# Optimization experiments

Hardware: AMD Instinct MI355X
Metric: run time of the kernel (lower is better)

Reference implementation:

```python
import jax, jax.numpy as jnp
import numpy as np

LENGTH, D, CHI, CLASSES = 784, 2, 128, 10
BATCH = 1024


def setup_inputs() -> dict:
    key = jax.random.key(0)
    k1, k2, k3 = jax.random.split(key, 3)
    # feature-mapped samples (batch, d, length), values in [0,1] like cossin map
    x = jax.random.uniform(k1, (BATCH, D, LENGTH), dtype=jnp.float32)
    # per-site residual weights; small init so the residual recurrence stays stable
    W = jax.random.normal(k2, (LENGTH, D, CHI, CHI), dtype=jnp.float32) * (0.01 / np.sqrt(CHI))
    # classifier matrix applied to the final hidden vector
    V = jax.random.normal(k3, (CHI, CLASSES), dtype=jnp.float32) / np.sqrt(CHI)
    return {"x": x, "W": W, "V": V}


def reference(x, W, V):
    # x: (B, d, L), W: (L, d, chi, chi), V: (chi, classes)
    B = x.shape[0]
    chi = W.shape[2]
    h0 = jnp.ones((B, chi), dtype=x.dtype)  # initial hidden bond vector

    xs = jnp.moveaxis(x, 2, 0)  # (L, B, d) so scan iterates over sites

    def site_step(h, inputs):
        xn, Wn = inputs  # xn: (B, d), Wn: (d, chi, chi)
        # residual MPS update: h <- h + sum_{s,a} x[n,s] W_n[s,a,b] h[a]
        h = h + jnp.einsum('ns,sab,na->nb', xn, Wn, h)
        return h, None

    h, _ = jax.lax.scan(site_step, h0, (xs, W))
    logits = h @ V  # (B, classes)
    return logits
```

## Files before the change

kernel.cpp:

```cpp
#include <hip/hip_runtime.h>

#define LL 784
#define CHI 128
#define CLS 10
#define BC 16
#define NBLK 64

typedef __attribute__((ext_vector_type(8))) short short8;
typedef __attribute__((ext_vector_type(4))) float floatx4;

__device__ inline unsigned int f2bf(float v) {
    unsigned int u = __float_as_uint(v);
    u += 0x7fffu + ((u >> 16) & 1u);
    return u >> 16;
}

__device__ inline void lds_barrier() {
    asm volatile("s_waitcnt lgkmcnt(0)\n\ts_barrier" ::: "memory");
}

__device__ inline unsigned int cvt_pk_bf16(float lo, float hi) {
    unsigned int r;
    asm("v_cvt_pk_bf16_f32 %0, %1, %2" : "=v"(r) : "v"(lo), "v"(hi));
    return r;
}

template <int OFF>
__device__ inline short8 gload(const char* p) {
    short8 r;
    asm volatile("global_load_dwordx4 %0, %1, off offset:%2"
                 : "=v"(r) : "v"(p), "i"(OFF));
    return r;
}

__device__ inline floatx4 gloadf4(const float* p) {
    floatx4 r;
    asm volatile("global_load_dwordx4 %0, %1, off"
                 : "=v"(r) : "v"(p));
    return r;
}

__device__ inline void vm_wait24() {
    asm volatile("s_waitcnt vmcnt(24)" ::: "memory");
    __builtin_amdgcn_sched_barrier(0);
}
__device__ inline void vm_wait16() {
    asm volatile("s_waitcnt vmcnt(16)" ::: "memory");
    __builtin_amdgcn_sched_barrier(0);
}
__device__ inline void vm_wait8() {
    asm volatile("s_waitcnt vmcnt(8)" ::: "memory");
    __builtin_amdgcn_sched_barrier(0);
}
__device__ inline void vm_wait0() {
    asm volatile("s_waitcnt vmcnt(0)" ::: "memory");
    __builtin_amdgcn_sched_barrier(0);
}

__global__ __launch_bounds__(256) void prep_kernel(const float* __restrict__ W,
                                                   uint4* __restrict__ ws4) {
    __shared__ float tile[32 * 132];
    const int b = blockIdx.x;
    const int n = b >> 3, s = (b >> 2) & 1, kt = b & 3;
    const float* Wp = W + ((size_t)(n * 2 + s) * CHI + kt * 32) * CHI;
    const int t = threadIdx.x;
    #pragma unroll
    for (int k = 0; k < 4; k++) {
        int v = t + k * 256;
        int a = v >> 5, c4 = v & 31;
        float4 val = *(const float4*)(Wp + a * CHI + c4 * 4);
        *(float4*)&tile[a * 132 + c4 * 4] = val;
    }
    __syncthreads();
    const int l = t & 63, f0 = t >> 6;
    const int m_ = l & 15, q_ = l >> 4;
    #pragma unroll
    for (int ff = 0; ff < 2; ff++) {
        int nt = f0 + ff * 4;
        const float* tp = &tile[(q_ * 8) * 132 + nt * 16 + m_];
        uint4 pk;
        pk.x = f2bf(tp[0 * 132]) | (f2bf(tp[1 * 132]) << 16);
        pk.y = f2bf(tp[2 * 132]) | (f2bf(tp[3 * 132]) << 16);
        pk.z = f2bf(tp[4 * 132]) | (f2bf(tp[5 * 132]) << 16);
        pk.w = f2bf(tp[6 * 132]) | (f2bf(tp[7 * 132]) << 16);
        ws4[(size_t)(((n * 8 + nt) * 2 + s) * 4 + kt) * 64 + l] = pk;
    }
}

__global__ __launch_bounds__(512) void mps_kernel(const float* __restrict__ x,
                                                  const unsigned short* __restrict__ ws,
                                                  const float* __restrict__ V,
                                                  float* __restrict__ out) {
    __shared__ short8 bfbuf[2][4][64];
    __shared__ float hfin[BC * 136];

    const int t = threadIdx.x;
    const int w = t >> 6, l = t & 63;
    const int m = l & 15, q = l >> 4;
    const int rb = blockIdx.x * BC;

    for (int i = t; i < 1024; i += 512)
        ((unsigned int*)&bfbuf[0][0][0])[i] = 0x3F803F80u;

    const float* xp0 = x + (size_t)(rb + m) * (2 * LL);
    const float* xp1 = xp0 + LL;
    floatx4 xA0, xA1, xA2, xA3, xB0, xB1, xB2, xB3;
    xA0 = gloadf4(xp0 + 0);  xA1 = gloadf4(xp0 + 4);
    xA2 = gloadf4(xp1 + 0);  xA3 = gloadf4(xp1 + 4);

    const char* wsb = (const char*)ws + (size_t)w * 8192 + (size_t)l * 16;

    short8 bWA[8], bWB[8], bWC[8], bWD[8];
#define LOAD_BATCH(BUF, PTR) do {                                   \
    const char* p_ = (PTR);                                         \
    BUF[0] = gload<0>(p_);           BUF[1] = gload<1024>(p_);      \
    BUF[2] = gload<2048>(p_);        BUF[3] = gload<3072>(p_);      \
    BUF[4] = gload<0>(p_ + 4096);    BUF[5] = gload<1024>(p_ + 4096); \
    BUF[6] = gload<2048>(p_ + 4096); BUF[7] = gload<3072>(p_ + 4096); \
} while (0)

    LOAD_BATCH(bWA, wsb);
    LOAD_BATCH(bWB, wsb + 1 * 65536);
    LOAD_BATCH(bWC, wsb + 2 * 65536);
    LOAD_BATCH(bWD, wsb + 3 * 65536);

    floatx4 hacc = (floatx4){1.f, 1.f, 1.f, 1.f};

    unsigned int* const bfw = (unsigned int*)&bfbuf[0][0][0];
    const int wr_dw = (w >> 1) * 256 + (m + 16 * ((w & 1) * 2 + (q >> 1))) * 4 + (q & 1) * 2;

    __syncthreads();

#define SITE_BODY(NN, PAR, WBUF, X0, X1, PF, WAIT) do {                             \
    lds_barrier();                                                                  \
    short8 bf0 = bfbuf[PAR][0][l];                                                  \
    short8 bf1 = bfbuf[PAR][1][l];                                                  \
    short8 bf2 = bfbuf[PAR][2][l];                                                  \
    short8 bf3 = bfbuf[PAR][3][l];                                                  \
    WAIT();                                                                         \
    floatx4 z = (floatx4){0.f, 0.f, 0.f, 0.f};                                      \
    floatx4 p0 = __builtin_amdgcn_mfma_f32_16x16x32_bf16(WBUF[0], bf0, z, 0, 0, 0); \
    floatx4 p1 = __builtin_amdgcn_mfma_f32_16x16x32_bf16(WBUF[2], bf2, z, 0, 0, 0); \
    floatx4 q0 = __builtin_amdgcn_mfma_f32_16x16x32_bf16(WBUF[4], bf0, z, 0, 0, 0); \
    floatx4 q1 = __builtin_amdgcn_mfma_f32_16x16x32_bf16(WBUF[6], bf2, z, 0, 0, 0); \
    p0 = __builtin_amdgcn_mfma_f32_16x16x32_bf16(WBUF[1], bf1, p0, 0, 0, 0);        \
    p1 = __builtin_amdgcn_mfma_f32_16x16x32_bf16(WBUF[3], bf3, p1, 0, 0, 0);        \
    q0 = __builtin_amdgcn_mfma_f32_16x16x32_bf16(WBUF[5], bf1, q0, 0, 0, 0);        \
    q1 = __builtin_amdgcn_mfma_f32_16x16x32_bf16(WBUF[7], bf3, q1, 0, 0, 0);        \
    if (PF) LOAD_BATCH(WBUF, wsb + (size_t)((NN) + 4) * 65536);                     \
    _Pragma("unroll")                                                               \
    for (int i = 0; i < 4; i++)                                                     \
        hacc[i] += (X0) * (p0[i] + p1[i]) + (X1) * (q0[i] + q1[i]);                 \
    uint2 pk;                                                                       \
    pk.x = cvt_pk_bf16(hacc[0], hacc[1]);                                           \
    pk.y = cvt_pk_bf16(hacc[2], hacc[3]);                                           \
    *(uint2*)&bfw[((PAR) ^ 1) * 1024 + wr_dw] = pk;                                 \
} while (0)

    for (int nb = 0; nb < LL - 16; nb += 16) {
        xB0 = gloadf4(xp0 + nb + 8);
        xB1 = gloadf4(xp0 + nb + 12);
        xB2 = gloadf4(xp1 + nb + 8);
        xB3 = gloadf4(xp1 + nb + 12);
        SITE_BODY(nb + 0,  0, bWA, xA0[0], xA2[0], 1, vm_wait24);
        SITE_BODY(nb + 1,  1, bWB, xA0[1], xA2[1], 1, vm_wait24);
        SITE_BODY(nb + 2,  0, bWC, xA0[2], xA2[2], 1, vm_wait24);
        SITE_BODY(nb + 3,  1, bWD, xA0[3], xA2[3], 1, vm_wait24);
        SITE_BODY(nb + 4,  0, bWA, xA1[0], xA3[0], 1, vm_wait24);
        SITE_BODY(nb + 5,  1, bWB, xA1[1], xA3[1], 1, vm_wait24);
        SITE_BODY(nb + 6,  0, bWC, xA1[2], xA3[2], 1, vm_wait24);
        SITE_BODY(nb + 7,  1, bWD, xA1[3], xA3[3], 1, vm_wait24);
        xA0 = gloadf4(xp0 + nb + 16);
        xA1 = gloadf4(xp0 + nb + 20);
        xA2 = gloadf4(xp1 + nb + 16);
        xA3 = gloadf4(xp1 + nb + 20);
        SITE_BODY(nb + 8,  0, bWA, xB0[0], xB2[0], 1, vm_wait24);
        SITE_BODY(nb + 9,  1, bWB, xB0[1], xB2[1], 1, vm_wait24);
        SITE_BODY(nb + 10, 0, bWC, xB0[2], xB2[2], 1, vm_wait24);
        SITE_BODY(nb + 11, 1, bWD, xB0[3], xB2[3], 1, vm_wait24);
        SITE_BODY(nb + 12, 0, bWA, xB1[0], xB3[0], 1, vm_wait24);
        SITE_BODY(nb + 13, 1, bWB, xB1[1], xB3[1], 1, vm_wait24);
        SITE_BODY(nb + 14, 0, bWC, xB1[2], xB3[2], 1, vm_wait24);
        SITE_BODY(nb + 15, 1, bWD, xB1[3], xB3[3], 1, vm_wait24);
    }

    xB0 = gloadf4(xp0 + 768 + 8);
    xB1 = gloadf4(xp0 + 768 + 12);
    xB2 = gloadf4(xp1 + 768 + 8);
    xB3 = gloadf4(xp1 + 768 + 12);
    SITE_BODY(768, 0, bWA, xA0[0], xA2[0], 1, vm_wait24);
    SITE_BODY(769, 1, bWB, xA0[1], xA2[1], 1, vm_wait24);
    SITE_BODY(770, 0, bWC, xA0[2], xA2[2], 1, vm_wait24);
    SITE_BODY(771, 1, bWD, xA0[3], xA2[3], 1, vm_wait24);
    SITE_BODY(772, 0, bWA, xA1[0], xA3[0], 1, vm_wait24);
    SITE_BODY(773, 1, bWB, xA1[1], xA3[1], 1, vm_wait24);
    SITE_BODY(774, 0, bWC, xA1[2], xA3[2], 1, vm_wait24);
    SITE_BODY(775, 1, bWD, xA1[3], xA3[3], 1, vm_wait24);
    SITE_BODY(776, 0, bWA, xB0[0], xB2[0], 1, vm_wait24);
    SITE_BODY(777, 1, bWB, xB0[1], xB2[1], 1, vm_wait24);
    SITE_BODY(778, 0, bWC, xB0[2], xB2[2], 1, vm_wait24);
    SITE_BODY(779, 1, bWD, xB0[3], xB2[3], 1, vm_wait24);
    SITE_BODY(780, 0, bWA, xB1[0], xB3[0], 0, vm_wait24);
    SITE_BODY(781, 1, bWB, xB1[1], xB3[1], 0, vm_wait16);
    SITE_BODY(782, 0, bWC, xB1[2], xB3[2], 0, vm_wait8);
    SITE_BODY(783, 1, bWD, xB1[3], xB3[3], 0, vm_wait0);
#undef SITE_BODY
#undef LOAD_BATCH

    *(floatx4*)&hfin[m * 136 + w * 16 + q * 4] = hacc;
    __syncthreads();

    if (t < BC * CLS) {
        int r = t / CLS, cls = t % CLS;
        float sum = 0.f;
        for (int a = 0; a < CHI; a++) sum += hfin[r * 136 + a] * V[a * CLS + cls];
        out[(size_t)(rb + r) * CLS + cls] = sum;
    }
}

extern "C" void kernel_launch(void* const* d_in, const int* in_sizes, int n_in,
                              void* d_out, int out_size, void* d_ws, size_t ws_size,
                              hipStream_t stream) {
    const float* x = (const float*)d_in[0];
    const float* W = (const float*)d_in[1];
    const float* V = (const float*)d_in[2];
    float* out = (float*)d_out;

    prep_kernel<<<LL * 8, 256, 0, stream>>>(W, (uint4*)d_ws);
    mps_kernel<<<NBLK, 512, 0, stream>>>(x, (const unsigned short*)d_ws, V, out);
}
```

Measured before the change: 682.5 us.

## Process 32 batch rows per block, sharing each site's weight loads across two tiles

Each block now handles two 16-row batch tiles, so every weight fragment loaded from global memory feeds twice as many MFMAs. The grid halves from 64 to 32 blocks. The weight prefetch depth drops from four sites to two, which frees registers for the second accumulator and x buffers. The trade-off is that only half as many CUs are busy, each with longer per-site compute, and the shallower prefetch leaves less time to hide weight-load latency on the serial recurrence.

Result: slower. 843.7 us (+23.6%).

```diff
diff --git a/kernel.cpp b/kernel.cpp
--- a/kernel.cpp
+++ b/kernel.cpp
@@ -3,8 +3,8 @@
 #define LL 784
 #define CHI 128
 #define CLS 10
-#define BC 16
-#define NBLK 64
+#define BC 32
+#define NBLK 32
 
 typedef __attribute__((ext_vector_type(8))) short short8;
 typedef __attribute__((ext_vector_type(4))) float floatx4;
@@ -40,14 +40,6 @@
     return r;
 }
 
-__device__ inline void vm_wait24() {
-    asm volatile("s_waitcnt vmcnt(24)" ::: "memory");
-    __builtin_amdgcn_sched_barrier(0);
-}
-__device__ inline void vm_wait16() {
-    asm volatile("s_waitcnt vmcnt(16)" ::: "memory");
-    __builtin_amdgcn_sched_barrier(0);
-}
 __device__ inline void vm_wait8() {
     asm volatile("s_waitcnt vmcnt(8)" ::: "memory");
     __builtin_amdgcn_sched_barrier(0);
@@ -91,7 +83,7 @@
                                                   const unsigned short* __restrict__ ws,
                                                   const float* __restrict__ V,
                                                   float* __restrict__ out) {
-    __shared__ short8 bfbuf[2][4][64];
+    __shared__ short8 bfbuf[2][4][2][64];
     __shared__ float hfin[BC * 136];
 
     const int t = threadIdx.x;
@@ -99,18 +91,23 @@
     const int m = l & 15, q = l >> 4;
     const int rb = blockIdx.x * BC;
 
-    for (int i = t; i < 1024; i += 512)
-        ((unsigned int*)&bfbuf[0][0][0])[i] = 0x3F803F80u;
+    for (int i = t; i < 2048; i += 512)
+        ((unsigned int*)&bfbuf[0][0][0][0])[i] = 0x3F803F80u;
 
     const float* xp0 = x + (size_t)(rb + m) * (2 * LL);
     const float* xp1 = xp0 + LL;
+    const float* xp2 = x + (size_t)(rb + 16 + m) * (2 * LL);
+    const float* xp3 = xp2 + LL;
     floatx4 xA0, xA1, xA2, xA3, xB0, xB1, xB2, xB3;
+    floatx4 xC0, xC1, xC2, xC3, xD0, xD1, xD2, xD3;
     xA0 = gloadf4(xp0 + 0);  xA1 = gloadf4(xp0 + 4);
     xA2 = gloadf4(xp1 + 0);  xA3 = gloadf4(xp1 + 4);
+    xC0 = gloadf4(xp2 + 0);  xC1 = gloadf4(xp2 + 4);
+    xC2 = gloadf4(xp3 + 0);  xC3 = gloadf4(xp3 + 4);
 
     const char* wsb = (const char*)ws + (size_t)w * 8192 + (size_t)l * 16;
 
-    short8 bWA[8], bWB[8], bWC[8], bWD[8];
+    short8 bWA[8], bWB[8];
 #define LOAD_BATCH(BUF, PTR) do {                                   \
     const char* p_ = (PTR);                                         \
     BUF[0] = gload<0>(p_);           BUF[1] = gload<1024>(p_);      \
@@ -120,41 +117,58 @@
 } while (0)
 
     LOAD_BATCH(bWA, wsb);
-    LOAD_BATCH(bWB, wsb + 1 * 65536);
-    LOAD_BATCH(bWC, wsb + 2 * 65536);
-    LOAD_BATCH(bWD, wsb + 3 * 65536);
-
-    floatx4 hacc = (floatx4){1.f, 1.f, 1.f, 1.f};
-
-    unsigned int* const bfw = (unsigned int*)&bfbuf[0][0][0];
-    const int wr_dw = (w >> 1) * 256 + (m + 16 * ((w & 1) * 2 + (q >> 1))) * 4 + (q & 1) * 2;
+    LOAD_BATCH(bWB, wsb + 65536);
+
+    floatx4 hacc0 = (floatx4){1.f, 1.f, 1.f, 1.f};
+    floatx4 hacc1 = (floatx4){1.f, 1.f, 1.f, 1.f};
+
+    unsigned int* const bfw = (unsigned int*)&bfbuf[0][0][0][0];
+    const int l2 = m + 16 * ((w & 1) * 2 + (q >> 1));
+    const int wr_dw = ((w >> 1) * 2) * 256 + l2 * 4 + (q & 1) * 2;
 
     __syncthreads();
 
-#define SITE_BODY(NN, PAR, WBUF, X0, X1, PF, WAIT) do {                             \
-    lds_barrier();                                                                  \
-    short8 bf0 = bfbuf[PAR][0][l];                                                  \
-    short8 bf1 = bfbuf[PAR][1][l];                                                  \
-    short8 bf2 = bfbuf[PAR][2][l];                                                  \
-    short8 bf3 = bfbuf[PAR][3][l];                                                  \
-    WAIT();                                                                         \
-    floatx4 z = (floatx4){0.f, 0.f, 0.f, 0.f};                                      \
-    floatx4 p0 = __builtin_amdgcn_mfma_f32_16x16x32_bf16(WBUF[0], bf0, z, 0, 0, 0); \
-    floatx4 p1 = __builtin_amdgcn_mfma_f32_16x16x32_bf16(WBUF[2], bf2, z, 0, 0, 0); \
-    floatx4 q0 = __builtin_amdgcn_mfma_f32_16x16x32_bf16(WBUF[4], bf0, z, 0, 0, 0); \
-    floatx4 q1 = __builtin_amdgcn_mfma_f32_16x16x32_bf16(WBUF[6], bf2, z, 0, 0, 0); \
-    p0 = __builtin_amdgcn_mfma_f32_16x16x32_bf16(WBUF[1], bf1, p0, 0, 0, 0);        \
-    p1 = __builtin_amdgcn_mfma_f32_16x16x32_bf16(WBUF[3], bf3, p1, 0, 0, 0);        \
-    q0 = __builtin_amdgcn_mfma_f32_16x16x32_bf16(WBUF[5], bf1, q0, 0, 0, 0);        \
-    q1 = __builtin_amdgcn_mfma_f32_16x16x32_bf16(WBUF[7], bf3, q1, 0, 0, 0);        \
-    if (PF) LOAD_BATCH(WBUF, wsb + (size_t)((NN) + 4) * 65536);                     \
-    _Pragma("unroll")                                                               \
-    for (int i = 0; i < 4; i++)                                                     \
-        hacc[i] += (X0) * (p0[i] + p1[i]) + (X1) * (q0[i] + q1[i]);                 \
-    uint2 pk;                                                                       \
-    pk.x = cvt_pk_bf16(hacc[0], hacc[1]);                                           \
-    pk.y = cvt_pk_bf16(hacc[2], hacc[3]);                                           \
-    *(uint2*)&bfw[((PAR) ^ 1) * 1024 + wr_dw] = pk;                                 \
+#define SITE_BODY(NN, PAR, WBUF, X0, X1, X2, X3, PF, WAIT) do {                       \
+    lds_barrier();                                                                    \
+    short8 bf00 = bfbuf[PAR][0][0][l];                                                \
+    short8 bf10 = bfbuf[PAR][1][0][l];                                                \
+    short8 bf20 = bfbuf[PAR][2][0][l];                                                \
+    short8 bf30 = bfbuf[PAR][3][0][l];                                                \
+    short8 bf01 = bfbuf[PAR][0][1][l];                                                \
+    short8 bf11 = bfbuf[PAR][1][1][l];                                                \
+    short8 bf21 = bfbuf[PAR][2][1][l];                                                \
+    short8 bf31 = bfbuf[PAR][3][1][l];                                                \
+    WAIT();                                                                           \
+    floatx4 z = (floatx4){0.f, 0.f, 0.f, 0.f};                                        \
+    floatx4 pA0 = __builtin_amdgcn_mfma_f32_16x16x32_bf16(WBUF[0], bf00, z, 0, 0, 0); \
+    floatx4 pA1 = __builtin_amdgcn_mfma_f32_16x16x32_bf16(WBUF[2], bf20, z, 0, 0, 0); \
+    floatx4 qA0 = __builtin_amdgcn_mfma_f32_16x16x32_bf16(WBUF[4], bf00, z, 0, 0, 0); \
+    floatx4 qA1 = __builtin_amdgcn_mfma_f32_16x16x32_bf16(WBUF[6], bf20, z, 0, 0, 0); \
+    floatx4 pB0 = __builtin_amdgcn_mfma_f32_16x16x32_bf16(WBUF[0], bf01, z, 0, 0, 0); \
+    floatx4 pB1 = __builtin_amdgcn_mfma_f32_16x16x32_bf16(WBUF[2], bf21, z, 0, 0, 0); \
+    floatx4 qB0 = __builtin_amdgcn_mfma_f32_16x16x32_bf16(WBUF[4], bf01, z, 0, 0, 0); \
+    floatx4 qB1 = __builtin_amdgcn_mfma_f32_16x16x32_bf16(WBUF[6], bf21, z, 0, 0, 0); \
+    pA0 = __builtin_amdgcn_mfma_f32_16x16x32_bf16(WBUF[1], bf10, pA0, 0, 0, 0);       \
+    pA1 = __builtin_amdgcn_mfma_f32_16x16x32_bf16(WBUF[3], bf30, pA1, 0, 0, 0);       \
+    qA0 = __builtin_amdgcn_mfma_f32_16x16x32_bf16(WBUF[5], bf10, qA0, 0, 0, 0);       \
+    qA1 = __builtin_amdgcn_mfma_f32_16x16x32_bf16(WBUF[7], bf30, qA1, 0, 0, 0);       \
+    pB0 = __builtin_amdgcn_mfma_f32_16x16x32_bf16(WBUF[1], bf11, pB0, 0, 0, 0);       \
+    pB1 = __builtin_amdgcn_mfma_f32_16x16x32_bf16(WBUF[3], bf31, pB1, 0, 0, 0);       \
+    qB0 = __builtin_amdgcn_mfma_f32_16x16x32_bf16(WBUF[5], bf11, qB0, 0, 0, 0);       \
+    qB1 = __builtin_amdgcn_mfma_f32_16x16x32_bf16(WBUF[7], bf31, qB1, 0, 0, 0);       \
+    if (PF) LOAD_BATCH(WBUF, wsb + (size_t)((NN) + 2) * 65536);                       \
+    _Pragma("unroll")                                                                 \
+    for (int i = 0; i < 4; i++) {                                                     \
+        hacc0[i] += (X0) * (pA0[i] + pA1[i]) + (X1) * (qA0[i] + qA1[i]);              \
+        hacc1[i] += (X2) * (pB0[i] + pB1[i]) + (X3) * (qB0[i] + qB1[i]);              \
+    }                                                                                 \
+    uint2 pk0, pk1;                                                                   \
+    pk0.x = cvt_pk_bf16(hacc0[0], hacc0[1]);                                          \
+    pk0.y = cvt_pk_bf16(hacc0[2], hacc0[3]);                                          \
+    pk1.x = cvt_pk_bf16(hacc1[0], hacc1[1]);                                          \
+    pk1.y = cvt_pk_bf16(hacc1[2], hacc1[3]);                                          \
+    *(uint2*)&bfw[((PAR) ^ 1) * 2048 + wr_dw]       = pk0;                            \
+    *(uint2*)&bfw[((PAR) ^ 1) * 2048 + 256 + wr_dw] = pk1;                            \
 } while (0)
 
     for (int nb = 0; nb < LL - 16; nb += 16) {
@@ -162,52 +176,65 @@
         xB1 = gloadf4(xp0 + nb + 12);
         xB2 = gloadf4(xp1 + nb + 8);
         xB3 = gloadf4(xp1 + nb + 12);
-        SITE_BODY(nb + 0,  0, bWA, xA0[0], xA2[0], 1, vm_wait24);
-        SITE_BODY(nb + 1,  1, bWB, xA0[1], xA2[1], 1, vm_wait24);
-        SITE_BODY(nb + 2,  0, bWC, xA0[2], xA2[2], 1, vm_wait24);
-        SITE_BODY(nb + 3,  1, bWD, xA0[3], xA2[3], 1, vm_wait24);
-        SITE_BODY(nb + 4,  0, bWA, xA1[0], xA3[0], 1, vm_wait24);
-        SITE_BODY(nb + 5,  1, bWB, xA1[1], xA3[1], 1, vm_wait24);
-        SITE_BODY(nb + 6,  0, bWC, xA1[2], xA3[2], 1, vm_wait24);
-        SITE_BODY(nb + 7,  1, bWD, xA1[3], xA3[3], 1, vm_wait24);
+        xD0 = gloadf4(xp2 + nb + 8);
+        xD1 = gloadf4(xp2 + nb + 12);
+        xD2 = gloadf4(xp3 + nb + 8);
+        xD3 = gloadf4(xp3 + nb + 12);
+        SITE_BODY(nb + 0,  0, bWA, xA0[0], xA2[0], xC0[0], xC2[0], 1, vm_wait8);
+        SITE_BODY(nb + 1,  1, bWB, xA0[1], xA2[1], xC0[1], xC2[1], 1, vm_wait8);
+        SITE_BODY(nb + 2,  0, bWA, xA0[2], xA2[2], xC0[2], xC2[2], 1, vm_wait8);
+        SITE_BODY(nb + 3,  1, bWB, xA0[3], xA2[3], xC0[3], xC2[3], 1, vm_wait8);
+        SITE_BODY(nb + 4,  0, bWA, xA1[0], xA3[0], xC1[0], xC3[0], 1, vm_wait8);
+        SITE_BODY(nb + 5,  1, bWB, xA1[1], xA3[1], xC1[1], xC3[1], 1, vm_wait8);
+        SITE_BODY(nb + 6,  0, bWA, xA1[2], xA3[2], xC1[2], xC3[2], 1, vm_wait8);
+        SITE_BODY(nb + 7,  1, bWB, xA1[3], xA3[3], xC1[3], xC3[3], 1, vm_wait8);
         xA0 = gloadf4(xp0 + nb + 16);
         xA1 = gloadf4(xp0 + nb + 20);
         xA2 = gloadf4(xp1 + nb + 16);
         xA3 = gloadf4(xp1 + nb + 20);
-        SITE_BODY(nb + 8,  0, bWA, xB0[0], xB2[0], 1, vm_wait24);
-        SITE_BODY(nb + 9,  1, bWB, xB0[1], xB2[1], 1, vm_wait24);
-        SITE_BODY(nb + 10, 0, bWC, xB0[2], xB2[2], 1, vm_wait24);
-        SITE_BODY(nb + 11, 1, bWD, xB0[3], xB2[3], 1, vm_wait24);
-        SITE_BODY(nb + 12, 0, bWA, xB1[0], xB3[0], 1, vm_wait24);
-        SITE_BODY(nb + 13, 1, bWB, xB1[1], xB3[1], 1, vm_wait24);
-        SITE_BODY(nb + 14, 0, bWC, xB1[2], xB3[2], 1, vm_wait24);
-        SITE_BODY(nb + 15, 1, bWD, xB1[3], xB3[3], 1, vm_wait24);
+        xC0 = gloadf4(xp2 + nb + 16);
+        xC1 = gloadf4(xp2 + nb + 20);
+        xC2 = gloadf4(xp3 + nb + 16);
+        xC3 = gloadf4(xp3 + nb + 20);
+        SITE_BODY(nb + 8,  0, bWA, xB0[0], xB2[0], xD0[0], xD2[0], 1, vm_wait8);
+        SITE_BODY(nb + 9,  1, bWB, xB0[1], xB2[1], xD0[1], xD2[1], 1, vm_wait8);
+        SITE_BODY(nb + 10, 0, bWA, xB0[2], xB2[2], xD0[2], xD2[2], 1, vm_wait8);
+        SITE_BODY(nb + 11, 1, bWB, xB0[3], xB2[3], xD0[3], xD2[3], 1, vm_wait8);
+        SITE_BODY(nb + 12, 0, bWA, xB1[0], xB3[0], xD1[0], xD3[0], 1, vm_wait8);
+        SITE_BODY(nb + 13, 1, bWB, xB1[1], xB3[1], xD1[1], xD3[1], 1, vm_wait8);
+        SITE_BODY(nb + 14, 0, bWA, xB1[2], xB3[2], xD1[2], xD3[2], 1, vm_wait8);
+        SITE_BODY(nb + 15, 1, bWB, xB1[3], xB3[3], xD1[3], xD3[3], 1, vm_wait8);
     }
 
     xB0 = gloadf4(xp0 + 768 + 8);
     xB1 = gloadf4(xp0 + 768 + 12);
     xB2 = gloadf4(xp1 + 768 + 8);
     xB3 = gloadf4(xp1 + 768 + 12);
-    SITE_BODY(768, 0, bWA, xA0[0], xA2[0], 1, vm_wait24);
-    SITE_BODY(769, 1, bWB, xA0[1], xA2[1], 1, vm_wait24);
-    SITE_BODY(770, 0, bWC, xA0[2], xA2[2], 1, vm_wait24);
-    SITE_BODY(771, 1, bWD, xA0[3], xA2[3], 1, vm_wait24);
-    SITE_BODY(772, 0, bWA, xA1[0], xA3[0], 1, vm_wait24);
-    SITE_BODY(773, 1, bWB, xA1[1], xA3[1], 1, vm_wait24);
-    SITE_BODY(774, 0, bWC, xA1[2], xA3[2], 1, vm_wait24);
-    SITE_BODY(775, 1, bWD, xA1[3], xA3[3], 1, vm_wait24);
-    SITE_BODY(776, 0, bWA, xB0[0], xB2[0], 1, vm_wait24);
-    SITE_BODY(777, 1, bWB, xB0[1], xB2[1], 1, vm_wait24);
-    SITE_BODY(778, 0, bWC, xB0[2], xB2[2], 1, vm_wait24);
-    SITE_BODY(779, 1, bWD, xB0[3], xB2[3], 1, vm_wait24);
-    SITE_BODY(780, 0, bWA, xB1[0], xB3[0], 0, vm_wait24);
-    SITE_BODY(781, 1, bWB, xB1[1], xB3[1], 0, vm_wait16);
-    SITE_BODY(782, 0, bWC, xB1[2], xB3[2], 0, vm_wait8);
-    SITE_BODY(783, 1, bWD, xB1[3], xB3[3], 0, vm_wait0);
+    xD0 = gloadf4(xp2 + 768 + 8);
+    xD1 = gloadf4(xp2 + 768 + 12);
+    xD2 = gloadf4(xp3 + 768 + 8);
+    xD3 = gloadf4(xp3 + 768 + 12);
+    SITE_BODY(768, 0, bWA, xA0[0], xA2[0], xC0[0], xC2[0], 1, vm_wait8);
+    SITE_BODY(769, 1, bWB, xA0[1], xA2[1], xC0[1], xC2[1], 1, vm_wait8);
+    SITE_BODY(770, 0, bWA, xA0[2], xA2[2], xC0[2], xC2[2], 1, vm_wait8);
+    SITE_BODY(771, 1, bWB, xA0[3], xA2[3], xC0[3], xC2[3], 1, vm_wait8);
+    SITE_BODY(772, 0, bWA, xA1[0], xA3[0], xC1[0], xC3[0], 1, vm_wait8);
+    SITE_BODY(773, 1, bWB, xA1[1], xA3[1], xC1[1], xC3[1], 1, vm_wait8);
+    SITE_BODY(774, 0, bWA, xA1[2], xA3[2], xC1[2], xC3[2], 1, vm_wait8);
+    SITE_BODY(775, 1, bWB, xA1[3], xA3[3], xC1[3], xC3[3], 1, vm_wait8);
+    SITE_BODY(776, 0, bWA, xB0[0], xB2[0], xD0[0], xD2[0], 1, vm_wait8);
+    SITE_BODY(777, 1, bWB, xB0[1], xB2[1], xD0[1], xD2[1], 1, vm_wait8);
+    SITE_BODY(778, 0, bWA, xB0[2], xB2[2], xD0[2], xD2[2], 1, vm_wait8);
+    SITE_BODY(779, 1, bWB, xB0[3], xB2[3], xD0[3], xD2[3], 1, vm_wait8);
+    SITE_BODY(780, 0, bWA, xB1[0], xB3[0], xD1[0], xD3[0], 1, vm_wait8);
+    SITE_BODY(781, 1, bWB, xB1[1], xB3[1], xD1[1], xD3[1], 1, vm_wait8);
+    SITE_BODY(782, 0, bWA, xB1[2], xB3[2], xD1[2], xD3[2], 0, vm_wait8);
+    SITE_BODY(783, 1, bWB, xB1[3], xB3[3], xD1[3], xD3[3], 0, vm_wait0);
 #undef SITE_BODY
 #undef LOAD_BATCH
 
-    *(floatx4*)&hfin[m * 136 + w * 16 + q * 4] = hacc;
+    *(floatx4*)&hfin[m * 136 + w * 16 + q * 4]        = hacc0;
+    *(floatx4*)&hfin[(m + 16) * 136 + w * 16 + q * 4] = hacc1;
     __syncthreads();
 
     if (t < BC * CLS) {
```

## Switch recurrence matmuls to FP8 MFMA with residual decomposition around ones

Applied to the files above, without the earlier changes.

Quantizes W (scaled by 256) to FP8 E4M3 and stores h as FP8 offsets from the all-ones start vector (scaled by 16). The ones contribution is handled exactly through precomputed column sums R produced by a new prep kernel. Each site now uses eight FP8 MFMAs with half-size weight loads and a two-deep prefetch instead of four. This halves weight bandwidth and register footprint. In exchange it adds software FP8 conversion on the critical path, one more kernel, and more quantization error.

Result: slower. 774.9 us (+13.5%).

```diff
diff --git a/kernel.cpp b/kernel.cpp
--- a/kernel.cpp
+++ b/kernel.cpp
@@ -6,33 +6,43 @@
 #define BC 16
 #define NBLK 64
 
-typedef __attribute__((ext_vector_type(8))) short short8;
 typedef __attribute__((ext_vector_type(4))) float floatx4;
-
-__device__ inline unsigned int f2bf(float v) {
+typedef __attribute__((ext_vector_type(2))) long lng2;
+
+__device__ inline unsigned int f2fp8(float v) {
     unsigned int u = __float_as_uint(v);
-    u += 0x7fffu + ((u >> 16) & 1u);
-    return u >> 16;
+    unsigned int s = (u >> 24) & 0x80u;
+    unsigned int a = u & 0x7fffffffu;
+    if (a >= 0x43e00000u) return s | 0x7Eu;
+    if (a <  0x3c800000u) return s;
+    unsigned int r = a + 0x0007ffffu + ((a >> 20) & 1u);
+    if (r >= 0x43e00000u) return s | 0x7Eu;
+    unsigned int E = (r >> 23) - 120u;
+    return s | (E << 3) | ((r >> 20) & 7u);
+}
+
+__device__ inline unsigned int pk4_fp8(float v0, float v1, float v2, float v3) {
+    return f2fp8(v0) | (f2fp8(v1) << 8) | (f2fp8(v2) << 16) | (f2fp8(v3) << 24);
 }
 
 __device__ inline void lds_barrier() {
     asm volatile("s_waitcnt lgkmcnt(0)\n\ts_barrier" ::: "memory");
 }
 
-__device__ inline unsigned int cvt_pk_bf16(float lo, float hi) {
-    unsigned int r;
-    asm("v_cvt_pk_bf16_f32 %0, %1, %2" : "=v"(r) : "v"(lo), "v"(hi));
-    return r;
-}
-
 template <int OFF>
-__device__ inline short8 gload(const char* p) {
-    short8 r;
+__device__ inline lng2 gload16(const char* p) {
+    lng2 r;
     asm volatile("global_load_dwordx4 %0, %1, off offset:%2"
                  : "=v"(r) : "v"(p), "i"(OFF));
     return r;
 }
-
+template <int OFF>
+__device__ inline floatx4 gloadf4o(const float* p) {
+    floatx4 r;
+    asm volatile("global_load_dwordx4 %0, %1, off offset:%2"
+                 : "=v"(r) : "v"(p), "i"(OFF));
+    return r;
+}
 __device__ inline floatx4 gloadf4(const float* p) {
     floatx4 r;
     asm volatile("global_load_dwordx4 %0, %1, off"
@@ -40,16 +50,12 @@
     return r;
 }
 
-__device__ inline void vm_wait24() {
-    asm volatile("s_waitcnt vmcnt(24)" ::: "memory");
+__device__ inline void vm_wait10() {
+    asm volatile("s_waitcnt vmcnt(10)" ::: "memory");
     __builtin_amdgcn_sched_barrier(0);
 }
-__device__ inline void vm_wait16() {
-    asm volatile("s_waitcnt vmcnt(16)" ::: "memory");
-    __builtin_amdgcn_sched_barrier(0);
-}
-__device__ inline void vm_wait8() {
-    asm volatile("s_waitcnt vmcnt(8)" ::: "memory");
+__device__ inline void vm_wait6() {
+    asm volatile("s_waitcnt vmcnt(6)" ::: "memory");
     __builtin_amdgcn_sched_barrier(0);
 }
 __device__ inline void vm_wait0() {
@@ -58,7 +64,7 @@
 }
 
 __global__ __launch_bounds__(256) void prep_kernel(const float* __restrict__ W,
-                                                   uint4* __restrict__ ws4) {
+                                                   unsigned char* __restrict__ ws8) {
     __shared__ float tile[32 * 132];
     const int b = blockIdx.x;
     const int n = b >> 3, s = (b >> 2) & 1, kt = b & 3;
@@ -74,24 +80,39 @@
     __syncthreads();
     const int l = t & 63, f0 = t >> 6;
     const int m_ = l & 15, q_ = l >> 4;
+    const int f = s * 4 + kt;
     #pragma unroll
     for (int ff = 0; ff < 2; ff++) {
         int nt = f0 + ff * 4;
         const float* tp = &tile[(q_ * 8) * 132 + nt * 16 + m_];
-        uint4 pk;
-        pk.x = f2bf(tp[0 * 132]) | (f2bf(tp[1 * 132]) << 16);
-        pk.y = f2bf(tp[2 * 132]) | (f2bf(tp[3 * 132]) << 16);
-        pk.z = f2bf(tp[4 * 132]) | (f2bf(tp[5 * 132]) << 16);
-        pk.w = f2bf(tp[6 * 132]) | (f2bf(tp[7 * 132]) << 16);
-        ws4[(size_t)(((n * 8 + nt) * 2 + s) * 4 + kt) * 64 + l] = pk;
-    }
+        unsigned int dw0 = pk4_fp8(tp[0 * 132] * 256.f, tp[1 * 132] * 256.f,
+                                   tp[2 * 132] * 256.f, tp[3 * 132] * 256.f);
+        unsigned int dw1 = pk4_fp8(tp[4 * 132] * 256.f, tp[5 * 132] * 256.f,
+                                   tp[6 * 132] * 256.f, tp[7 * 132] * 256.f);
+        size_t addr = (size_t)n * 32768 + (size_t)nt * 4096 + (f >> 1) * 1024
+                    + l * 16 + (f & 1) * 8;
+        uint2 pk; pk.x = dw0; pk.y = dw1;
+        *(uint2*)(ws8 + addr) = pk;
+    }
+}
+
+__global__ __launch_bounds__(256) void prepR_kernel(const float* __restrict__ W,
+                                                    float* __restrict__ R) {
+    const int n = blockIdx.x, t = threadIdx.x;
+    const int s = t >> 7, c = t & 127;
+    const float* Wp = W + ((size_t)(n * 2 + s) * CHI) * CHI + c;
+    float sum = 0.f;
+    #pragma unroll 8
+    for (int a = 0; a < CHI; a++) sum += Wp[(size_t)a * CHI];
+    R[(n * 2 + s) * CHI + c] = sum;
 }
 
 __global__ __launch_bounds__(512) void mps_kernel(const float* __restrict__ x,
-                                                  const unsigned short* __restrict__ ws,
+                                                  const unsigned char* __restrict__ ws8,
+                                                  const float* __restrict__ R,
                                                   const float* __restrict__ V,
                                                   float* __restrict__ out) {
-    __shared__ short8 bfbuf[2][4][64];
+    __shared__ long bfb[2][4][64];
     __shared__ float hfin[BC * 136];
 
     const int t = threadIdx.x;
@@ -99,8 +120,7 @@
     const int m = l & 15, q = l >> 4;
     const int rb = blockIdx.x * BC;
 
-    for (int i = t; i < 1024; i += 512)
-        ((unsigned int*)&bfbuf[0][0][0])[i] = 0x3F803F80u;
+    for (int i = t; i < 256; i += 512) ((long*)bfb)[i] = 0L;
 
     const float* xp0 = x + (size_t)(rb + m) * (2 * LL);
     const float* xp1 = xp0 + LL;
@@ -108,53 +128,56 @@
     xA0 = gloadf4(xp0 + 0);  xA1 = gloadf4(xp0 + 4);
     xA2 = gloadf4(xp1 + 0);  xA3 = gloadf4(xp1 + 4);
 
-    const char* wsb = (const char*)ws + (size_t)w * 8192 + (size_t)l * 16;
-
-    short8 bWA[8], bWB[8], bWC[8], bWD[8];
-#define LOAD_BATCH(BUF, PTR) do {                                   \
-    const char* p_ = (PTR);                                         \
-    BUF[0] = gload<0>(p_);           BUF[1] = gload<1024>(p_);      \
-    BUF[2] = gload<2048>(p_);        BUF[3] = gload<3072>(p_);      \
-    BUF[4] = gload<0>(p_ + 4096);    BUF[5] = gload<1024>(p_ + 4096); \
-    BUF[6] = gload<2048>(p_ + 4096); BUF[7] = gload<3072>(p_ + 4096); \
+    const char* wsb = (const char*)ws8 + (size_t)w * 4096 + (size_t)l * 16;
+    const float* rbase = R + w * 16 + q * 4;
+
+    lng2 bWA[4], bWB[4];
+    floatx4 rA0, rA1, rB0, rB1;
+#define LOAD_BATCH(WB_, R0_, R1_, NT_) do {                         \
+    const char* p_ = wsb + (size_t)(NT_) * 32768;                   \
+    WB_[0] = gload16<0>(p_);     WB_[1] = gload16<1024>(p_);        \
+    WB_[2] = gload16<2048>(p_);  WB_[3] = gload16<3072>(p_);        \
+    const float* rp_ = rbase + (NT_) * 256;                         \
+    R0_ = gloadf4o<0>(rp_);  R1_ = gloadf4o<512>(rp_);              \
 } while (0)
 
-    LOAD_BATCH(bWA, wsb);
-    LOAD_BATCH(bWB, wsb + 1 * 65536);
-    LOAD_BATCH(bWC, wsb + 2 * 65536);
-    LOAD_BATCH(bWD, wsb + 3 * 65536);
+    LOAD_BATCH(bWA, rA0, rA1, 0);
+    LOAD_BATCH(bWB, rB0, rB1, 1);
 
     floatx4 hacc = (floatx4){1.f, 1.f, 1.f, 1.f};
 
-    unsigned int* const bfw = (unsigned int*)&bfbuf[0][0][0];
-    const int wr_dw = (w >> 1) * 256 + (m + 16 * ((w & 1) * 2 + (q >> 1))) * 4 + (q & 1) * 2;
+    unsigned int* const bfw = (unsigned int*)&bfb[0][0][0];
+    const int wr_dw = (w >> 1) * 128 + (m + 16 * ((w & 1) * 2 + (q >> 1))) * 2 + (q & 1);
 
     __syncthreads();
 
-#define SITE_BODY(NN, PAR, WBUF, X0, X1, PF, WAIT) do {                             \
+#define MFMA8(A, B, C) __builtin_amdgcn_mfma_f32_16x16x32_fp8_fp8((A), (B), (C), 0, 0, 0)
+
+#define SITE_BODY(NN, PAR, WBUF, RB0_, RB1_, X0, X1, PF, WAIT) do {                 \
     lds_barrier();                                                                  \
-    short8 bf0 = bfbuf[PAR][0][l];                                                  \
-    short8 bf1 = bfbuf[PAR][1][l];                                                  \
-    short8 bf2 = bfbuf[PAR][2][l];                                                  \
-    short8 bf3 = bfbuf[PAR][3][l];                                                  \
+    long d0 = bfb[PAR][0][l];                                                       \
+    long d1 = bfb[PAR][1][l];                                                       \
+    long d2 = bfb[PAR][2][l];                                                       \
+    long d3 = bfb[PAR][3][l];                                                       \
     WAIT();                                                                         \
+    floatx4 r0 = RB0_, r1 = RB1_;                \
     floatx4 z = (floatx4){0.f, 0.f, 0.f, 0.f};                                      \
-    floatx4 p0 = __builtin_amdgcn_mfma_f32_16x16x32_bf16(WBUF[0], bf0, z, 0, 0, 0); \
-    floatx4 p1 = __builtin_amdgcn_mfma_f32_16x16x32_bf16(WBUF[2], bf2, z, 0, 0, 0); \
-    floatx4 q0 = __builtin_amdgcn_mfma_f32_16x16x32_bf16(WBUF[4], bf0, z, 0, 0, 0); \
-    floatx4 q1 = __builtin_amdgcn_mfma_f32_16x16x32_bf16(WBUF[6], bf2, z, 0, 0, 0); \
-    p0 = __builtin_amdgcn_mfma_f32_16x16x32_bf16(WBUF[1], bf1, p0, 0, 0, 0);        \
-    p1 = __builtin_amdgcn_mfma_f32_16x16x32_bf16(WBUF[3], bf3, p1, 0, 0, 0);        \
-    q0 = __builtin_amdgcn_mfma_f32_16x16x32_bf16(WBUF[5], bf1, q0, 0, 0, 0);        \
-    q1 = __builtin_amdgcn_mfma_f32_16x16x32_bf16(WBUF[7], bf3, q1, 0, 0, 0);        \
-    if (PF) LOAD_BATCH(WBUF, wsb + (size_t)((NN) + 4) * 65536);                     \
+    floatx4 p0 = MFMA8(WBUF[0][0], d0, z);                                          \
+    floatx4 p1 = MFMA8(WBUF[2][0], d0, z);                                          \
+    p0 = MFMA8(WBUF[0][1], d1, p0);                                                 \
+    p1 = MFMA8(WBUF[2][1], d1, p1);                                                 \
+    p0 = MFMA8(WBUF[1][0], d2, p0);                                                 \
+    p1 = MFMA8(WBUF[3][0], d2, p1);                                                 \
+    p0 = MFMA8(WBUF[1][1], d3, p0);                                                 \
+    p1 = MFMA8(WBUF[3][1], d3, p1);                                                 \
+    if (PF) LOAD_BATCH(WBUF, RB0_, RB1_, (NN) + 2);                                 \
+    float X0s = (X0) * 2.44140625e-4f, X1s = (X1) * 2.44140625e-4f;                 \
     _Pragma("unroll")                                                               \
     for (int i = 0; i < 4; i++)                                                     \
-        hacc[i] += (X0) * (p0[i] + p1[i]) + (X1) * (q0[i] + q1[i]);                 \
-    uint2 pk;                                                                       \
-    pk.x = cvt_pk_bf16(hacc[0], hacc[1]);                                           \
-    pk.y = cvt_pk_bf16(hacc[2], hacc[3]);                                           \
-    *(uint2*)&bfw[((PAR) ^ 1) * 1024 + wr_dw] = pk;                                 \
+        hacc[i] += (X0) * r0[i] + (X1) * r1[i] + X0s * p0[i] + X1s * p1[i];         \
+    float e0 = hacc[0] * 16.f - 16.f, e1 = hacc[1] * 16.f - 16.f;                   \
+    float e2 = hacc[2] * 16.f - 16.f, e3 = hacc[3] * 16.f - 16.f;                   \
+    bfw[((PAR) ^ 1) * 512 + wr_dw] = pk4_fp8(e0, e1, e2, e3);                       \
 } while (0)
 
     for (int nb = 0; nb < LL - 16; nb += 16) {
@@ -162,50 +185,51 @@
         xB1 = gloadf4(xp0 + nb + 12);
         xB2 = gloadf4(xp1 + nb + 8);
         xB3 = gloadf4(xp1 + nb + 12);
-        SITE_BODY(nb + 0,  0, bWA, xA0[0], xA2[0], 1, vm_wait24);
-        SITE_BODY(nb + 1,  1, bWB, xA0[1], xA2[1], 1, vm_wait24);
-        SITE_BODY(nb + 2,  0, bWC, xA0[2], xA2[2], 1, vm_wait24);
-        SITE_BODY(nb + 3,  1, bWD, xA0[3], xA2[3], 1, vm_wait24);
-        SITE_BODY(nb + 4,  0, bWA, xA1[0], xA3[0], 1, vm_wait24);
-        SITE_BODY(nb + 5,  1, bWB, xA1[1], xA3[1], 1, vm_wait24);
-        SITE_BODY(nb + 6,  0, bWC, xA1[2], xA3[2], 1, vm_wait24);
-        SITE_BODY(nb + 7,  1, bWD, xA1[3], xA3[3], 1, vm_wait24);
+        SITE_BODY(nb + 0,  0, bWA, rA0, rA1, xA0[0], xA2[0], 1, vm_wait10);
+        SITE_BODY(nb + 1,  1, bWB, rB0, rB1, xA0[1], xA2[1], 1, vm_wait6);
+        SITE_BODY(nb + 2,  0, bWA, rA0, rA1, xA0[2], xA2[2], 1, vm_wait6);
+        SITE_BODY(nb + 3,  1, bWB, rB0, rB1, xA0[3], xA2[3], 1, vm_wait6);
+        SITE_BODY(nb + 4,  0, bWA, rA0, rA1, xA1[0], xA3[0], 1, vm_wait6);
+        SITE_BODY(nb + 5,  1, bWB, rB0, rB1, xA1[1], xA3[1], 1, vm_wait6);
+        SITE_BODY(nb + 6,  0, bWA, rA0, rA1, xA1[2], xA3[2], 1, vm_wait6);
+        SITE_BODY(nb + 7,  1, bWB, rB0, rB1, xA1[3], xA3[3], 1, vm_wait6);
         xA0 = gloadf4(xp0 + nb + 16);
         xA1 = gloadf4(xp0 + nb + 20);
         xA2 = gloadf4(xp1 + nb + 16);
         xA3 = gloadf4(xp1 + nb + 20);
-        SITE_BODY(nb + 8,  0, bWA, xB0[0], xB2[0], 1, vm_wait24);
-        SITE_BODY(nb + 9,  1, bWB, xB0[1], xB2[1], 1, vm_wait24);
-        SITE_BODY(nb + 10, 0, bWC, xB0[2], xB2[2], 1, vm_wait24);
-        SITE_BODY(nb + 11, 1, bWD, xB0[3], xB2[3], 1, vm_wait24);
-        SITE_BODY(nb + 12, 0, bWA, xB1[0], xB3[0], 1, vm_wait24);
-        SITE_BODY(nb + 13, 1, bWB, xB1[1], xB3[1], 1, vm_wait24);
-        SITE_BODY(nb + 14, 0, bWC, xB1[2], xB3[2], 1, vm_wait24);
-        SITE_BODY(nb + 15, 1, bWD, xB1[3], xB3[3], 1, vm_wait24);
+        SITE_BODY(nb + 8,  0, bWA, rA0, rA1, xB0[0], xB2[0], 1, vm_wait10);
+        SITE_BODY(nb + 9,  1, bWB, rB0, rB1, xB0[1], xB2[1], 1, vm_wait6);
+        SITE_BODY(nb + 10, 0, bWA, rA0, rA1, xB0[2], xB2[2], 1, vm_wait6);
+        SITE_BODY(nb + 11, 1, bWB, rB0, rB1, xB0[3], xB2[3], 1, vm_wait6);
+        SITE_BODY(nb + 12, 0, bWA, rA0, rA1, xB1[0], xB3[0], 1, vm_wait6);
+        SITE_BODY(nb + 13, 1, bWB, rB0, rB1, xB1[1], xB3[1], 1, vm_wait6);
+        SITE_BODY(nb + 14, 0, bWA, rA0, rA1, xB1[2], xB3[2], 1, vm_wait6);
+        SITE_BODY(nb + 15, 1, bWB, rB0, rB1, xB1[3], xB3[3], 1, vm_wait6);
     }
 
     xB0 = gloadf4(xp0 + 768 + 8);
     xB1 = gloadf4(xp0 + 768 + 12);
     xB2 = gloadf4(xp1 + 768 + 8);
     xB3 = gloadf4(xp1 + 768 + 12);
-    SITE_BODY(768, 0, bWA, xA0[0], xA2[0], 1, vm_wait24);
-    SITE_BODY(769, 1, bWB, xA0[1], xA2[1], 1, vm_wait24);
-    SITE_BODY(770, 0, bWC, xA0[2], xA2[2], 1, vm_wait24);
-    SITE_BODY(771, 1, bWD, xA0[3], xA2[3], 1, vm_wait24);
-    SITE_BODY(772, 0, bWA, xA1[0], xA3[0], 1, vm_wait24);
-    SITE_BODY(773, 1, bWB, xA1[1], xA3[1], 1, vm_wait24);
-    SITE_BODY(774, 0, bWC, xA1[2], xA3[2], 1, vm_wait24);
-    SITE_BODY(775, 1, bWD, xA1[3], xA3[3], 1, vm_wait24);
-    SITE_BODY(776, 0, bWA, xB0[0], xB2[0], 1, vm_wait24);
-    SITE_BODY(777, 1, bWB, xB0[1], xB2[1], 1, vm_wait24);
-    SITE_BODY(778, 0, bWC, xB0[2], xB2[2], 1, vm_wait24);
-    SITE_BODY(779, 1, bWD, xB0[3], xB2[3], 1, vm_wait24);
-    SITE_BODY(780, 0, bWA, xB1[0], xB3[0], 0, vm_wait24);
-    SITE_BODY(781, 1, bWB, xB1[1], xB3[1], 0, vm_wait16);
-    SITE_BODY(782, 0, bWC, xB1[2], xB3[2], 0, vm_wait8);
-    SITE_BODY(783, 1, bWD, xB1[3], xB3[3], 0, vm_wait0);
+    SITE_BODY(768, 0, bWA, rA0, rA1, xA0[0], xA2[0], 1, vm_wait10);
+    SITE_BODY(769, 1, bWB, rB0, rB1, xA0[1], xA2[1], 1, vm_wait6);
+    SITE_BODY(770, 0, bWA, rA0, rA1, xA0[2], xA2[2], 1, vm_wait6);
+    SITE_BODY(771, 1, bWB, rB0, rB1, xA0[3], xA2[3], 1, vm_wait6);
+    SITE_BODY(772, 0, bWA, rA0, rA1, xA1[0], xA3[0], 1, vm_wait6);
+    SITE_BODY(773, 1, bWB, rB0, rB1, xA1[1], xA3[1], 1, vm_wait6);
+    SITE_BODY(774, 0, bWA, rA0, rA1, xA1[2], xA3[2], 1, vm_wait6);
+    SITE_BODY(775, 1, bWB, rB0, rB1, xA1[3], xA3[3], 1, vm_wait6);
+    SITE_BODY(776, 0, bWA, rA0, rA1, xB0[0], xB2[0], 1, vm_wait10);
+    SITE_BODY(777, 1, bWB, rB0, rB1, xB0[1], xB2[1], 1, vm_wait6);
+    SITE_BODY(778, 0, bWA, rA0, rA1, xB0[2], xB2[2], 1, vm_wait6);
+    SITE_BODY(779, 1, bWB, rB0, rB1, xB0[3], xB2[3], 1, vm_wait6);
+    SITE_BODY(780, 0, bWA, rA0, rA1, xB1[0], xB3[0], 1, vm_wait6);
+    SITE_BODY(781, 1, bWB, rB0, rB1, xB1[1], xB3[1], 1, vm_wait6);
+    SITE_BODY(782, 0, bWA, rA0, rA1, xB1[2], xB3[2], 0, vm_wait6);
+    SITE_BODY(783, 1, bWB, rB0, rB1, xB1[3], xB3[3], 0, vm_wait0);
 #undef SITE_BODY
 #undef LOAD_BATCH
+#undef MFMA8
 
     *(floatx4*)&hfin[m * 136 + w * 16 + q * 4] = hacc;
     __syncthreads();
@@ -226,6 +250,10 @@
     const float* V = (const float*)d_in[2];
     float* out = (float*)d_out;
 
-    prep_kernel<<<LL * 8, 256, 0, stream>>>(W, (uint4*)d_ws);
-    mps_kernel<<<NBLK, 512, 0, stream>>>(x, (const unsigned short*)d_ws, V, out);
-}
+    unsigned char* ws8 = (unsigned char*)d_ws;
+    float* R = (float*)(ws8 + (size_t)LL * 32768);
+
+    prep_kernel<<<LL * 8, 256, 0, stream>>>(W, ws8);
+    prepR_kernel<<<LL, 256, 0, stream>>>(W, R);
+    mps_kernel<<<NBLK, 512, 0, stream>>>(x, ws8, R, V, out);
+}
```
